# Kernel tuning notes

Measured on AMD Instinct MI355X. Metric: run time of the kernel, lower is better.

Reference implementation:

```python
import jax, jax.numpy as jnp
import numpy as np

D_MODEL = 1024
NUM_HEADS = 16
D_K = D_MODEL // NUM_HEADS
LN_EPS = 1e-5


def setup_inputs() -> dict:
    key = jax.random.key(0)
    ks = jax.random.split(key, 10)
    s = 1.0 / np.sqrt(D_MODEL)
    x = jax.random.normal(ks[0], (4, 2048, D_MODEL), dtype=jnp.float32)
    Wq = jax.random.normal(ks[1], (D_MODEL, D_MODEL), dtype=jnp.float32) * s
    bq = jnp.zeros((D_MODEL,), dtype=jnp.float32)
    Wk = jax.random.normal(ks[2], (D_MODEL, D_MODEL), dtype=jnp.float32) * s
    bk = jnp.zeros((D_MODEL,), dtype=jnp.float32)
    Wv = jax.random.normal(ks[3], (D_MODEL, D_MODEL), dtype=jnp.float32) * s
    bv = jnp.zeros((D_MODEL,), dtype=jnp.float32)
    Wo = jax.random.normal(ks[4], (D_MODEL, D_MODEL), dtype=jnp.float32) * s
    bo = jnp.zeros((D_MODEL,), dtype=jnp.float32)
    gamma = jnp.ones((D_MODEL,), dtype=jnp.float32)
    beta = jnp.zeros((D_MODEL,), dtype=jnp.float32)
    return {"x": x, "Wq": Wq, "bq": bq, "Wk": Wk, "bk": bk,
            "Wv": Wv, "bv": bv, "Wo": Wo, "bo": bo,
            "gamma": gamma, "beta": beta}


def reference(x, Wq, bq, Wk, bk, Wv, bv, Wo, bo, gamma, beta):
    # x: [b, s, d]; torch Linear: y = x @ W.T + b. Dropout is identity (eval).
    b, s, d = x.shape
    h, dk = NUM_HEADS, D_K

    def proj(W, bias):  # [b, s, h, dk] -> [b, h, s, dk]
        return (jnp.einsum('bsd,ed->bse', x, W) + bias).reshape(b, s, h, dk).transpose(0, 2, 1, 3)

    Q, K, V = proj(Wq, bq), proj(Wk, bk), proj(Wv, bv)
    scores = jnp.einsum('bhqk,bhsk->bhqs', Q, K) / jnp.sqrt(jnp.float32(dk))
    attn = jax.nn.softmax(scores, axis=-1)
    ctx = jnp.einsum('bhqs,bhsk->bhqk', attn, V)  # [b, h, s, dk]
    ctx = ctx.transpose(0, 2, 1, 3).reshape(b, s, d)
    out = jnp.einsum('bsd,ed->bse', ctx, Wo) + bo
    y = out + x  # residual
    mu = jnp.mean(y, axis=-1, keepdims=True)
    var = jnp.mean(jnp.square(y - mu), axis=-1, keepdims=True)
    return (y - mu) * jax.lax.rsqrt(var + LN_EPS) * gamma + beta
```

## Files before the change

kernel.cpp:

```cpp
#include <hip/hip_runtime.h>

typedef unsigned short u16;
typedef unsigned int   u32;
typedef float f32x4 __attribute__((ext_vector_type(4)));
typedef short s16x8 __attribute__((ext_vector_type(8)));
typedef u32 u32x4 __attribute__((ext_vector_type(4)));

#define D_MODEL 1024
#define NHEADS  16
#define DK      64
#define SEQ     2048
#define BATCH   4
#define MROWS   (BATCH * SEQ)

#define C2 0.18033688011112042f

#define FIXEDM 14.0f

#if __has_builtin(__builtin_amdgcn_exp2f)
#define EXP2(x) __builtin_amdgcn_exp2f(x)
#else
#define EXP2(x) exp2f(x)
#endif

#define GL16(gp, lp) __builtin_amdgcn_global_load_lds( \
    (const __attribute__((address_space(1))) u32*)(gp), \
    (__attribute__((address_space(3))) u32*)(lp), 16, 0, 0)

#define SBAR()   __builtin_amdgcn_s_barrier()
#define SCHEDB() __builtin_amdgcn_sched_barrier(0)
#define WAITV0() asm volatile("s_waitcnt vmcnt(0)" ::: "memory")
#define WAITV3() asm volatile("s_waitcnt vmcnt(3)" ::: "memory")
#define WAITV4() asm volatile("s_waitcnt vmcnt(4)" ::: "memory")

__device__ __forceinline__ u16 f2b(float f) {
    u32 u = __builtin_bit_cast(u32, f);
    u32 r = (u + 0x7fffu + ((u >> 16) & 1u)) >> 16;
    return (u16)r;
}
__device__ __forceinline__ u32 pack2_trunc(float a, float b) {
    return __builtin_amdgcn_perm(__builtin_bit_cast(u32, b),
                                 __builtin_bit_cast(u32, a), 0x07060302u);
}

__global__ __launch_bounds__(256)
void cvt_all(const float* __restrict__ x,  const float* __restrict__ wq,
             const float* __restrict__ wk, const float* __restrict__ wv,
             const float* __restrict__ wo,
             u16* __restrict__ xb, u16* __restrict__ wqb, u16* __restrict__ wkb,
             u16* __restrict__ wvb, u16* __restrict__ wob)
{
    const int i = blockIdx.x * 256 + threadIdx.x;
    const float* src; u16* dst; int off;
    if (i < 2097152) { src = x; dst = xb; off = i; }
    else {
        const int j = i - 2097152;
        const int w = j >> 18;
        off = j & 262143;
        if      (w == 0) { src = wq; dst = wqb; }
        else if (w == 1) { src = wk; dst = wkb; }
        else if (w == 2) { src = wv; dst = wvb; }
        else             { src = wo; dst = wob; }
    }
    const float4 v = reinterpret_cast<const float4*>(src)[off];
    u32 lo = (u32)f2b(v.x) | ((u32)f2b(v.y) << 16);
    u32 hi = (u32)f2b(v.z) | ((u32)f2b(v.w) << 16);
    reinterpret_cast<uint2*>(dst)[off] = make_uint2(lo, hi);
}

#define QBM 256
#define QBN 128
#define BK 32
#define KITER (D_MODEL / BK)

__global__ __launch_bounds__(512, 4)
void gemm_qkv(const u16* __restrict__ A,
              const u16* __restrict__ Wq, const u16* __restrict__ Wk,
              const u16* __restrict__ Wv,
              const float* __restrict__ bq, const float* __restrict__ bk,
              const float* __restrict__ bv,
              u16* __restrict__ Qb, u16* __restrict__ Kb, u16* __restrict__ VtB)
{
    __shared__ __align__(16) u16 As[2][8192];
    __shared__ __align__(16) u16 Bs[2][4096];
    const int t    = threadIdx.x;
    const int lane = t & 63;
    const int w    = t >> 6;
    const int wm = w >> 1, wn = w & 1;

    const int orig = blockIdx.x;
    const int wgid = (orig & 7) * 96 + (orig >> 3);
    const int bx = wgid % 24;
    const int by = wgid / 24;

    const int sel = bx >> 3;
    const int n0  = (bx & 7) * QBN;
    const int m0  = by * QBM;
    const int quad = lane >> 4;
    const int rlo  = lane & 15;

    const u16* W = (sel == 0) ? Wq : (sel == 1) ? Wk : Wv;
    const float* bias = (sel == 0) ? bq : (sel == 1) ? bk : bv;

    const int srow = w * 16 + rlo;
    const long aoff0 = (long)(m0 + srow) * D_MODEL + quad * 8;
    const long aoff1 = aoff0 + (long)128 * D_MODEL;
    const long boff  = (long)(n0 + srow) * D_MODEL + quad * 8;
    const int dstw = w * 512 + lane * 8;

    f32x4 acc[4][4];
    #pragma unroll
    for (int i = 0; i < 4; i++)
        #pragma unroll
        for (int j = 0; j < 4; j++)
            acc[i][j] = (f32x4){0.f, 0.f, 0.f, 0.f};

    GL16(A + aoff0, &As[0][dstw]);
    GL16(A + aoff1, &As[0][dstw + 4096]);
    GL16(W + boff,  &Bs[0][dstw]);
    GL16(A + aoff0 + BK, &As[1][dstw]);
    GL16(A + aoff1 + BK, &As[1][dstw + 4096]);
    GL16(W + boff + BK,  &Bs[1][dstw]);

    for (int it = 0; it < KITER; it++) {
        const int cur = it & 1;
        if (it + 1 < KITER) { WAITV3(); } else { WAITV0(); }
        SBAR();
        SCHEDB();
        s16x8 af[4], bf[4];
        #pragma unroll
        for (int i = 0; i < 4; i++)
            af[i] = *reinterpret_cast<const s16x8*>(&As[cur][(wm * 4 + i) * 512 + lane * 8]);
        #pragma unroll
        for (int j = 0; j < 4; j++)
            bf[j] = *reinterpret_cast<const s16x8*>(&Bs[cur][(wn * 4 + j) * 512 + lane * 8]);
        #pragma unroll
        for (int i = 0; i < 4; i++)
            #pragma unroll
            for (int j = 0; j < 4; j++)
                acc[i][j] = __builtin_amdgcn_mfma_f32_16x16x32_bf16(af[i], bf[j], acc[i][j], 0, 0, 0);
        SCHEDB();
        SBAR();
        if (it + 2 < KITER) {
            const int k0 = (it + 2) * BK;
            GL16(A + aoff0 + k0, &As[cur][dstw]);
            GL16(A + aoff1 + k0, &As[cur][dstw + 4096]);
            GL16(W + boff + k0,  &Bs[cur][dstw]);
        }
    }

    if (sel == 2) {
        #pragma unroll
        for (int i = 0; i < 4; i++) {
            #pragma unroll
            for (int j = 0; j < 4; j++) {
                const int gm0 = m0 + wm * 64 + i * 16 + quad * 4;
                const int gn  = n0 + wn * 64 + j * 16 + rlo;
                const float bvx = bias[gn];
                const int bb = gm0 >> 11, s = gm0 & 2047;
                const int hh = gn >> 6, d = gn & 63;
                uint2 wv2;
                wv2.x = (u32)f2b(acc[i][j][0] + bvx) | ((u32)f2b(acc[i][j][1] + bvx) << 16);
                wv2.y = (u32)f2b(acc[i][j][2] + bvx) | ((u32)f2b(acc[i][j][3] + bvx) << 16);
                *reinterpret_cast<uint2*>(VtB + ((long)((bb * 16 + hh) * 64 + d)) * 2048 + s) = wv2;
            }
        }
    } else {
        u16* outp = (sel == 0) ? Qb : Kb;
        const float scale = (sel == 0) ? C2 : 1.0f;
        #pragma unroll
        for (int i = 0; i < 4; i++)
            #pragma unroll
            for (int j = 0; j < 4; j++)
                #pragma unroll
                for (int r = 0; r < 4; r++) {
                    const int gm = m0 + wm * 64 + i * 16 + quad * 4 + r;
                    const int gn = n0 + wn * 64 + j * 16 + rlo;
                    outp[(long)gm * D_MODEL + gn] = f2b((acc[i][j][r] + bias[gn]) * scale);
                }
    }
}

#define BM 128
#define BN 128

__global__ __launch_bounds__(256, 3)
void gemm_o(const u16* __restrict__ A, const u16* __restrict__ W,
            const float* __restrict__ bias, const float* __restrict__ resid,
            float* __restrict__ outF)
{
    __shared__ __align__(16) u16 As[2][4096];
    __shared__ __align__(16) u16 Bs[2][4096];
    const int t    = threadIdx.x;
    const int lane = t & 63;
    const int wave = t >> 6;
    const int wr = wave >> 1, wc = wave & 1;
    const int n0  = blockIdx.x * BN;
    const int m0  = blockIdx.y * BM;
    const int quad = lane >> 4;
    const int rlo  = lane & 15;

    const int srow0 = wave * 16 + rlo;
    const int scol  = quad * 8;
    const long aoff0 = (long)(m0 + srow0) * D_MODEL + scol;
    const long aoff1 = aoff0 + (long)64 * D_MODEL;
    const long boff0 = (long)(n0 + srow0) * D_MODEL + scol;
    const long boff1 = boff0 + (long)64 * D_MODEL;
    const int dst = wave * 512 + lane * 8;

    f32x4 acc[4][4];
    #pragma unroll
    for (int i = 0; i < 4; i++)
        #pragma unroll
        for (int j = 0; j < 4; j++)
            acc[i][j] = (f32x4){0.f, 0.f, 0.f, 0.f};

    GL16(A + aoff0, &As[0][dst]);
    GL16(A + aoff1, &As[0][dst + 2048]);
    GL16(W + boff0, &Bs[0][dst]);
    GL16(W + boff1, &Bs[0][dst + 2048]);
    GL16(A + aoff0 + BK, &As[1][dst]);
    GL16(A + aoff1 + BK, &As[1][dst + 2048]);
    GL16(W + boff0 + BK, &Bs[1][dst]);
    GL16(W + boff1 + BK, &Bs[1][dst + 2048]);

    for (int it = 0; it < KITER; it++) {
        const int cur = it & 1;
        if (it + 1 < KITER) { WAITV4(); } else { WAITV0(); }
        SBAR();
        SCHEDB();
        s16x8 af[4], bf[4];
        #pragma unroll
        for (int i = 0; i < 4; i++)
            af[i] = *reinterpret_cast<const s16x8*>(&As[cur][(wr * 4 + i) * 512 + lane * 8]);
        #pragma unroll
        for (int j = 0; j < 4; j++)
            bf[j] = *reinterpret_cast<const s16x8*>(&Bs[cur][(wc * 4 + j) * 512 + lane * 8]);
        #pragma unroll
        for (int i = 0; i < 4; i++)
            #pragma unroll
            for (int j = 0; j < 4; j++)
                acc[i][j] = __builtin_amdgcn_mfma_f32_16x16x32_bf16(af[i], bf[j], acc[i][j], 0, 0, 0);
        SCHEDB();
        SBAR();
        if (it + 2 < KITER) {
            const int k0 = (it + 2) * BK;
            GL16(A + aoff0 + k0, &As[cur][dst]);
            GL16(A + aoff1 + k0, &As[cur][dst + 2048]);
            GL16(W + boff0 + k0, &Bs[cur][dst]);
            GL16(W + boff1 + k0, &Bs[cur][dst + 2048]);
        }
    }

    #pragma unroll
    for (int i = 0; i < 4; i++)
        #pragma unroll
        for (int j = 0; j < 4; j++)
            #pragma unroll
            for (int r = 0; r < 4; r++) {
                const int gm = m0 + wr * 64 + i * 16 + quad * 4 + r;
                const int gn = n0 + wc * 64 + j * 16 + rlo;
                outF[(long)gm * D_MODEL + gn] =
                    acc[i][j][r] + bias[gn] + resid[(long)gm * D_MODEL + gn];
            }
}

__global__ __launch_bounds__(256, 3)
void flash_attn_mfma(const u16* __restrict__ Qg, const u16* __restrict__ Kg,
                     const u16* __restrict__ VtG, u16* __restrict__ C)
{
    __shared__ __align__(16) u16 smem[20480];
    u16* KsB   = &smem[4096];
    u16* VtBuf = &smem[12288];

    const int t    = threadIdx.x;
    const int lane = t & 63;
    const int wave = t >> 6;
    const int quad = lane >> 4;
    const int rlo  = lane & 15;
    const int swz  = rlo << 2;
    const int qt = blockIdx.x, h = blockIdx.y, b = blockIdx.z;
    const long colbase = (long)h * DK;
    const long rowb    = (long)b * SEQ;
    const long qrow0   = rowb + (long)qt * 128;
    const u16* kg    = Kg + rowb * D_MODEL + colbase;
    const u16* vbase = VtG + (long)(b * 16 + h) * 64 * 2048;
    u16* myPs = &smem[wave * 1024];

    const long koff = (long)(wave * 16 + rlo) * D_MODEL + quad * 8;
    const long voff = (long)(wave * 16 + rlo) * 2048 + quad * 8;
    const int  dkv  = wave * 512 + lane * 8;

    GL16(kg + koff,         &KsB[dkv]);
    GL16(kg + koff + 32,    &KsB[dkv + 2048]);
    GL16(vbase + voff,      &VtBuf[dkv]);
    GL16(vbase + voff + 32, &VtBuf[dkv + 2048]);

    s16x8 bfq[2][2];
    #pragma unroll
    for (int mi = 0; mi < 2; mi++)
        #pragma unroll
        for (int ks = 0; ks < 2; ks++)
            bfq[mi][ks] = *reinterpret_cast<const s16x8*>(
                Qg + (qrow0 + wave * 32 + mi * 16 + rlo) * D_MODEL +
                colbase + ks * 32 + quad * 8);

    s16x8 ones;
    #pragma unroll
    for (int e = 0; e < 8; e++) ones[e] = (short)0x3F80;

    f32x4 o[2][4], o5[2];
    #pragma unroll
    for (int mi = 0; mi < 2; mi++) {
        o5[mi] = (f32x4){0.f, 0.f, 0.f, 0.f};
        #pragma unroll
        for (int db = 0; db < 4; db++)
            o[mi][db] = (f32x4){0.f, 0.f, 0.f, 0.f};
    }

    for (int kt = 0; kt < SEQ / 64; kt++) {
        const int cur = kt & 1;
        __syncthreads();
        if (kt + 1 < SEQ / 64) {
            const long kv0 = (long)(kt + 1) * 64;
            const int nb = cur ^ 1;
            GL16(kg + kv0 * D_MODEL + koff,      &KsB[nb * 4096 + dkv]);
            GL16(kg + kv0 * D_MODEL + koff + 32, &KsB[nb * 4096 + dkv + 2048]);
            GL16(vbase + kv0 + voff,             &VtBuf[nb * 4096 + dkv]);
            GL16(vbase + kv0 + voff + 32,        &VtBuf[nb * 4096 + dkv + 2048]);
        }
        const u16* Ks  = &KsB[cur * 4096];
        const u16* Vts = &VtBuf[cur * 4096];

        s16x8 afk[2][4], bfv[4][2];
        #pragma unroll
        for (int ks = 0; ks < 2; ks++)
            #pragma unroll
            for (int kb = 0; kb < 4; kb++)
                afk[ks][kb] = *reinterpret_cast<const s16x8*>(
                    &Ks[ks * 2048 + kb * 512 + lane * 8]);
        #pragma unroll
        for (int db = 0; db < 4; db++)
            #pragma unroll
            for (int ks = 0; ks < 2; ks++)
                bfv[db][ks] = *reinterpret_cast<const s16x8*>(
                    &Vts[ks * 2048 + db * 512 + lane * 8]);

        #pragma unroll
        for (int mi = 0; mi < 2; mi++) {
            f32x4 sc[4];
            #pragma unroll
            for (int kb = 0; kb < 4; kb++) sc[kb] = (f32x4){0.f, 0.f, 0.f, 0.f};
            #pragma unroll
            for (int ks = 0; ks < 2; ks++)
                #pragma unroll
                for (int kb = 0; kb < 4; kb++)
                    sc[kb] = __builtin_amdgcn_mfma_f32_16x16x32_bf16(
                        afk[ks][kb], bfq[mi][ks], sc[kb], 0, 0, 0);

            #pragma unroll
            for (int kb = 0; kb < 4; kb++) {
                float p0 = EXP2(sc[kb][0] - FIXEDM);
                float p1 = EXP2(sc[kb][1] - FIXEDM);
                float p2 = EXP2(sc[kb][2] - FIXEDM);
                float p3 = EXP2(sc[kb][3] - FIXEDM);
                uint2 wv2;
                wv2.x = pack2_trunc(p0, p1);
                wv2.y = pack2_trunc(p2, p3);
                *reinterpret_cast<uint2*>(
                    &myPs[rlo * 64 + ((kb * 16 + quad * 4) ^ swz)]) = wv2;
            }

            s16x8 afp[2];
            #pragma unroll
            for (int ks = 0; ks < 2; ks++) {
                const uint2 lo = *reinterpret_cast<const uint2*>(
                    &myPs[rlo * 64 + ((ks * 32 + quad * 8) ^ swz)]);
                const uint2 hi = *reinterpret_cast<const uint2*>(
                    &myPs[rlo * 64 + ((ks * 32 + quad * 8 + 4) ^ swz)]);
                u32x4 tv;
                tv.x = lo.x; tv.y = lo.y; tv.z = hi.x; tv.w = hi.y;
                afp[ks] = __builtin_bit_cast(s16x8, tv);
            }

            #pragma unroll
            for (int ks = 0; ks < 2; ks++) {
                #pragma unroll
                for (int db = 0; db < 4; db++)
                    o[mi][db] = __builtin_amdgcn_mfma_f32_16x16x32_bf16(
                        afp[ks], bfv[db][ks], o[mi][db], 0, 0, 0);
                o5[mi] = __builtin_amdgcn_mfma_f32_16x16x32_bf16(
                    afp[ks], ones, o5[mi], 0, 0, 0);
            }
        }
    }

    #pragma unroll
    for (int mi = 0; mi < 2; mi++)
        #pragma unroll
        for (int r = 0; r < 4; r++) {
            const float inv = 1.f / o5[mi][r];
            const long grow = qrow0 + wave * 32 + mi * 16 + quad * 4 + r;
            #pragma unroll
            for (int db = 0; db < 4; db++)
                C[grow * D_MODEL + colbase + db * 16 + rlo] = f2b(o[mi][db][r] * inv);
        }
}

__global__ __launch_bounds__(256)
void ln_inplace(float* __restrict__ Y, const float* __restrict__ gamma,
                const float* __restrict__ beta)
{
    const int row = blockIdx.x, t = threadIdx.x;
    float4 v = reinterpret_cast<float4*>(Y + (long)row * D_MODEL)[t];
    float s  = v.x + v.y + v.z + v.w;
    float ss = v.x * v.x + v.y * v.y + v.z * v.z + v.w * v.w;
    #pragma unroll
    for (int off = 32; off > 0; off >>= 1) {
        s  += __shfl_down(s, off, 64);
        ss += __shfl_down(ss, off, 64);
    }
    __shared__ float rs[4], rss[4];
    const int lane = t & 63, w = t >> 6;
    if (lane == 0) { rs[w] = s; rss[w] = ss; }
    __syncthreads();
    const float tot  = rs[0] + rs[1] + rs[2] + rs[3];
    const float tot2 = rss[0] + rss[1] + rss[2] + rss[3];
    const float mu   = tot * (1.f / D_MODEL);
    const float var  = tot2 * (1.f / D_MODEL) - mu * mu;
    const float rstd = rsqrtf(var + 1e-5f);
    const float4 g  = reinterpret_cast<const float4*>(gamma)[t];
    const float4 bb = reinterpret_cast<const float4*>(beta)[t];
    v.x = (v.x - mu) * rstd * g.x + bb.x;
    v.y = (v.y - mu) * rstd * g.y + bb.y;
    v.z = (v.z - mu) * rstd * g.z + bb.z;
    v.w = (v.w - mu) * rstd * g.w + bb.w;
    reinterpret_cast<float4*>(Y + (long)row * D_MODEL)[t] = v;
}

extern "C" void kernel_launch(void* const* d_in, const int* in_sizes, int n_in,
                              void* d_out, int out_size, void* d_ws, size_t ws_size,
                              hipStream_t stream)
{
    const float* x     = (const float*)d_in[0];
    const float* Wq    = (const float*)d_in[1];
    const float* bq    = (const float*)d_in[2];
    const float* Wk    = (const float*)d_in[3];
    const float* bk    = (const float*)d_in[4];
    const float* Wv    = (const float*)d_in[5];
    const float* bv    = (const float*)d_in[6];
    const float* Wo    = (const float*)d_in[7];
    const float* bo    = (const float*)d_in[8];
    const float* gamma = (const float*)d_in[9];
    const float* beta  = (const float*)d_in[10];
    float* out = (float*)d_out;

    u16* ws  = (u16*)d_ws;
    u16* xb  = ws;
    u16* Wqb = xb  + (size_t)MROWS * D_MODEL;
    u16* Wkb = Wqb + (size_t)D_MODEL * D_MODEL;
    u16* Wvb = Wkb + (size_t)D_MODEL * D_MODEL;
    u16* Wob = Wvb + (size_t)D_MODEL * D_MODEL;
    u16* Qb  = Wob + (size_t)D_MODEL * D_MODEL;
    u16* Kb  = Qb  + (size_t)MROWS * D_MODEL;
    u16* VtB = Kb  + (size_t)MROWS * D_MODEL;
    u16* Cb  = VtB + (size_t)MROWS * D_MODEL;

    cvt_all<<<12288, 256, 0, stream>>>(x, Wq, Wk, Wv, Wo, xb, Wqb, Wkb, Wvb, Wob);

    gemm_qkv<<<768, 512, 0, stream>>>(xb, Wqb, Wkb, Wvb, bq, bk, bv,
                                      Qb, Kb, VtB);

    flash_attn_mfma<<<dim3(SEQ / 128, NHEADS, BATCH), 256, 0, stream>>>(Qb, Kb, VtB, Cb);

    gemm_o<<<dim3(8, 64), 256, 0, stream>>>(Cb, Wob, bo, x, out);

    ln_inplace<<<MROWS, 256, 0, stream>>>(out, gamma, beta);
}
```

Baseline: 345.6 us.

## Fuse Q/K/V projections into one block sharing the A tile across three weights

Each QKV GEMM workgroup now computes the Q, K and V output tiles for the same row/column block. It loads the activation tile once and reuses it against three weight tiles, rather than launching separate blocks per projection that each reload A. This cuts global traffic for A by a factor of three and shrinks the grid from 768 to 256 blocks. In exchange it triples the accumulator registers, lowers the occupancy hint to 2, and enlarges LDS, which risks register pressure and a grid that may underfill the GPU's 256 CUs.

```diff
diff --git a/kernel.cpp b/kernel.cpp
--- a/kernel.cpp
+++ b/kernel.cpp
@@ -30,8 +30,8 @@
 #define SBAR()   __builtin_amdgcn_s_barrier()
 #define SCHEDB() __builtin_amdgcn_sched_barrier(0)
 #define WAITV0() asm volatile("s_waitcnt vmcnt(0)" ::: "memory")
-#define WAITV3() asm volatile("s_waitcnt vmcnt(3)" ::: "memory")
 #define WAITV4() asm volatile("s_waitcnt vmcnt(4)" ::: "memory")
+#define WAITV5() asm volatile("s_waitcnt vmcnt(5)" ::: "memory")
 
 __device__ __forceinline__ u16 f2b(float f) {
     u32 u = __builtin_bit_cast(u32, f);
@@ -68,12 +68,10 @@
     reinterpret_cast<uint2*>(dst)[off] = make_uint2(lo, hi);
 }
 
-#define QBM 256
-#define QBN 128
 #define BK 32
 #define KITER (D_MODEL / BK)
 
-__global__ __launch_bounds__(512, 4)
+__global__ __launch_bounds__(512, 2)
 void gemm_qkv(const u16* __restrict__ A,
               const u16* __restrict__ Wq, const u16* __restrict__ Wk,
               const u16* __restrict__ Wv,
@@ -82,25 +80,20 @@
               u16* __restrict__ Qb, u16* __restrict__ Kb, u16* __restrict__ VtB)
 {
     __shared__ __align__(16) u16 As[2][8192];
-    __shared__ __align__(16) u16 Bs[2][4096];
+    __shared__ __align__(16) u16 Bs[2][3][4096];
     const int t    = threadIdx.x;
     const int lane = t & 63;
     const int w    = t >> 6;
     const int wm = w >> 1, wn = w & 1;
 
     const int orig = blockIdx.x;
-    const int wgid = (orig & 7) * 96 + (orig >> 3);
-    const int bx = wgid % 24;
-    const int by = wgid / 24;
-
-    const int sel = bx >> 3;
-    const int n0  = (bx & 7) * QBN;
-    const int m0  = by * QBM;
+    const int wgid = (orig & 7) * 32 + (orig >> 3);
+    const int by = wgid >> 3;
+    const int bx = wgid & 7;
+    const int m0 = by * 256;
+    const int n0 = bx * 128;
     const int quad = lane >> 4;
     const int rlo  = lane & 15;
-
-    const u16* W = (sel == 0) ? Wq : (sel == 1) ? Wk : Wv;
-    const float* bias = (sel == 0) ? bq : (sel == 1) ? bk : bv;
 
     const int srow = w * 16 + rlo;
     const long aoff0 = (long)(m0 + srow) * D_MODEL + quad * 8;
@@ -108,77 +101,79 @@
     const long boff  = (long)(n0 + srow) * D_MODEL + quad * 8;
     const int dstw = w * 512 + lane * 8;
 
-    f32x4 acc[4][4];
-    #pragma unroll
-    for (int i = 0; i < 4; i++)
-        #pragma unroll
-        for (int j = 0; j < 4; j++)
-            acc[i][j] = (f32x4){0.f, 0.f, 0.f, 0.f};
+    f32x4 acc[3][4][4];
+    #pragma unroll
+    for (int s = 0; s < 3; s++)
+        #pragma unroll
+        for (int i = 0; i < 4; i++)
+            #pragma unroll
+            for (int j = 0; j < 4; j++)
+                acc[s][i][j] = (f32x4){0.f, 0.f, 0.f, 0.f};
 
     GL16(A + aoff0, &As[0][dstw]);
     GL16(A + aoff1, &As[0][dstw + 4096]);
-    GL16(W + boff,  &Bs[0][dstw]);
+    GL16(Wq + boff, &Bs[0][0][dstw]);
+    GL16(Wk + boff, &Bs[0][1][dstw]);
+    GL16(Wv + boff, &Bs[0][2][dstw]);
     GL16(A + aoff0 + BK, &As[1][dstw]);
     GL16(A + aoff1 + BK, &As[1][dstw + 4096]);
-    GL16(W + boff + BK,  &Bs[1][dstw]);
+    GL16(Wq + boff + BK, &Bs[1][0][dstw]);
+    GL16(Wk + boff + BK, &Bs[1][1][dstw]);
+    GL16(Wv + boff + BK, &Bs[1][2][dstw]);
 
     for (int it = 0; it < KITER; it++) {
         const int cur = it & 1;
-        if (it + 1 < KITER) { WAITV3(); } else { WAITV0(); }
+        if (it + 1 < KITER) { WAITV5(); } else { WAITV0(); }
         SBAR();
         SCHEDB();
-        s16x8 af[4], bf[4];
+        s16x8 af[4];
         #pragma unroll
         for (int i = 0; i < 4; i++)
             af[i] = *reinterpret_cast<const s16x8*>(&As[cur][(wm * 4 + i) * 512 + lane * 8]);
         #pragma unroll
-        for (int j = 0; j < 4; j++)
-            bf[j] = *reinterpret_cast<const s16x8*>(&Bs[cur][(wn * 4 + j) * 512 + lane * 8]);
-        #pragma unroll
-        for (int i = 0; i < 4; i++)
+        for (int s = 0; s < 3; s++) {
+            s16x8 bf[4];
             #pragma unroll
             for (int j = 0; j < 4; j++)
-                acc[i][j] = __builtin_amdgcn_mfma_f32_16x16x32_bf16(af[i], bf[j], acc[i][j], 0, 0, 0);
+                bf[j] = *reinterpret_cast<const s16x8*>(&Bs[cur][s][(wn * 4 + j) * 512 + lane * 8]);
+            #pragma unroll
+            for (int i = 0; i < 4; i++)
+                #pragma unroll
+                for (int j = 0; j < 4; j++)
+                    acc[s][i][j] = __builtin_amdgcn_mfma_f32_16x16x32_bf16(af[i], bf[j], acc[s][i][j], 0, 0, 0);
+        }
         SCHEDB();
         SBAR();
         if (it + 2 < KITER) {
             const int k0 = (it + 2) * BK;
             GL16(A + aoff0 + k0, &As[cur][dstw]);
             GL16(A + aoff1 + k0, &As[cur][dstw + 4096]);
-            GL16(W + boff + k0,  &Bs[cur][dstw]);
-        }
-    }
-
-    if (sel == 2) {
-        #pragma unroll
-        for (int i = 0; i < 4; i++) {
-            #pragma unroll
-            for (int j = 0; j < 4; j++) {
-                const int gm0 = m0 + wm * 64 + i * 16 + quad * 4;
-                const int gn  = n0 + wn * 64 + j * 16 + rlo;
-                const float bvx = bias[gn];
-                const int bb = gm0 >> 11, s = gm0 & 2047;
-                const int hh = gn >> 6, d = gn & 63;
-                uint2 wv2;
-                wv2.x = (u32)f2b(acc[i][j][0] + bvx) | ((u32)f2b(acc[i][j][1] + bvx) << 16);
-                wv2.y = (u32)f2b(acc[i][j][2] + bvx) | ((u32)f2b(acc[i][j][3] + bvx) << 16);
-                *reinterpret_cast<uint2*>(VtB + ((long)((bb * 16 + hh) * 64 + d)) * 2048 + s) = wv2;
+            GL16(Wq + boff + k0, &Bs[cur][0][dstw]);
+            GL16(Wk + boff + k0, &Bs[cur][1][dstw]);
+            GL16(Wv + boff + k0, &Bs[cur][2][dstw]);
+        }
+    }
+
+    #pragma unroll
+    for (int i = 0; i < 4; i++)
+        #pragma unroll
+        for (int j = 0; j < 4; j++) {
+            const int gm0 = m0 + wm * 64 + i * 16 + quad * 4;
+            const int gn  = n0 + wn * 64 + j * 16 + rlo;
+            const float bqx = bq[gn], bkx = bk[gn];
+            #pragma unroll
+            for (int r = 0; r < 4; r++) {
+                Qb[(long)(gm0 + r) * D_MODEL + gn] = f2b((acc[0][i][j][r] + bqx) * C2);
+                Kb[(long)(gm0 + r) * D_MODEL + gn] = f2b(acc[1][i][j][r] + bkx);
             }
-        }
-    } else {
-        u16* outp = (sel == 0) ? Qb : Kb;
-        const float scale = (sel == 0) ? C2 : 1.0f;
-        #pragma unroll
-        for (int i = 0; i < 4; i++)
-            #pragma unroll
-            for (int j = 0; j < 4; j++)
-                #pragma unroll
-                for (int r = 0; r < 4; r++) {
-                    const int gm = m0 + wm * 64 + i * 16 + quad * 4 + r;
-                    const int gn = n0 + wn * 64 + j * 16 + rlo;
-                    outp[(long)gm * D_MODEL + gn] = f2b((acc[i][j][r] + bias[gn]) * scale);
-                }
-    }
+            const float bvx = bv[gn];
+            const int bb = gm0 >> 11, s = gm0 & 2047;
+            const int hh = gn >> 6, d = gn & 63;
+            uint2 wv2;
+            wv2.x = (u32)f2b(acc[2][i][j][0] + bvx) | ((u32)f2b(acc[2][i][j][1] + bvx) << 16);
+            wv2.y = (u32)f2b(acc[2][i][j][2] + bvx) | ((u32)f2b(acc[2][i][j][3] + bvx) << 16);
+            *reinterpret_cast<uint2*>(VtB + ((long)((bb * 16 + hh) * 64 + d)) * 2048 + s) = wv2;
+        }
 }
 
 #define BM 128
@@ -468,7 +463,7 @@
 
     cvt_all<<<12288, 256, 0, stream>>>(x, Wq, Wk, Wv, Wo, xb, Wqb, Wkb, Wvb, Wob);
 
-    gemm_qkv<<<768, 512, 0, stream>>>(xb, Wqb, Wkb, Wvb, bq, bk, bv,
+    gemm_qkv<<<256, 512, 0, stream>>>(xb, Wqb, Wkb, Wvb, bq, bk, bv,
                                       Qb, Kb, VtB);
 
     flash_attn_mfma<<<dim3(SEQ / 128, NHEADS, BATCH), 256, 0, stream>>>(Qb, Kb, VtB, Cb);
```

New measurement: 329.3 us. -4.7%, faster.
